# Performance work log

Measured on AMD Instinct MI355X. Metric: run time of the kernel, lower is better.

Reference implementation:

```python
import jax, jax.numpy as jnp
import numpy as np

B, D, P, OUT = 16384, 1024, 1024, 25


def setup_inputs() -> dict:
    key = jax.random.key(0)
    ks = jax.random.split(key, 8)
    return {
        "patient_embed": jax.random.normal(ks[0], (B, D), jnp.float32),
        "prototype_embed": jax.random.normal(ks[1], (P, D), jnp.float32),
        "index": jax.random.permutation(ks[2], B),
        "bilinear_w": jax.random.normal(ks[3], (1, D, D), jnp.float32) * 0.02,
        "bilinear_b": jnp.zeros((1,), jnp.float32),
        "lin_w": jax.random.normal(ks[4], (1, 2 * D), jnp.float32) * 0.02,
        "proto_fc_w": jax.random.normal(ks[5], (P, D), jnp.float32) * 0.02,
        "proto_fc_b": jnp.zeros((P,), jnp.float32),
        "class_fc_w": jax.random.normal(ks[6], (OUT, P), jnp.float32) * 0.02,
        "class_fc_b": jnp.zeros((OUT,), jnp.float32),
    }


def reference(patient_embed, prototype_embed, index, bilinear_w, bilinear_b,
              lin_w, proto_fc_w, proto_fc_b, class_fc_w, class_fc_b):
    # prototype codebook is detached in the original (clone().detach())
    protos = jax.lax.stop_gradient(prototype_embed)  # [P, D]

    # cdist + argmin: nearest prototype per patient (VQ-style codebook lookup)
    e_sq = jnp.sum(patient_embed * patient_embed, axis=-1, keepdims=True)  # [B,1]
    p_sq = jnp.sum(protos * protos, axis=-1)[None, :]                      # [1,P]
    d2 = e_sq + p_sq - 2.0 * (patient_embed @ protos.T)                    # [B,P]
    dist = jnp.sqrt(jnp.maximum(d2, 0.0))
    labels_a = jnp.argmin(dist, axis=1)                                    # [B]

    # mixup partner via permutation; its nearest prototype is a gather of labels_a
    embed_b = patient_embed[index]
    labels_b = labels_a[index]

    pa = protos[labels_a]  # [B, D] prototype gather
    pb = protos[labels_b]

    # BiaffineAttention: bilinear(pa, pb) + lin(cat(pa, pb))
    bil = jnp.einsum('bi,oij,bj->bo', pa, bilinear_w, pb) + bilinear_b     # [B,1]
    lin = jnp.concatenate([pa, pb], axis=1) @ lin_w.T                      # [B,1]
    lam = jax.nn.sigmoid(bil + lin)                                        # [B,1]

    # adaptive mixup blend
    mixed_embed = lam * patient_embed + (1.0 - lam) * embed_b              # [B,D]

    # class_linear(mixed_embed) = class_fc(leaky_relu(proto_fc(mixed_embed)))
    proto_logits = mixed_embed @ proto_fc_w.T + proto_fc_b                 # [B,P]
    cls_logits = jax.nn.leaky_relu(proto_logits, 0.01) @ class_fc_w.T + class_fc_b  # [B,OUT]
    return cls_logits
```

## Files before the change

### kernel.cpp

```cpp
#include <hip/hip_runtime.h>
#include <math.h>

#define B_   16384
#define D_   1024
#define P_   1024
#define KS_  2048
#define OUT_ 25
#define NT_  48

typedef unsigned short u16;
typedef unsigned int   u32;
typedef unsigned long long u64;
typedef __attribute__((ext_vector_type(8))) short short8;
typedef __attribute__((ext_vector_type(4))) float f32x4;
typedef _Float16 half_t;
typedef __attribute__((ext_vector_type(2))) _Float16 h2;

struct alignas(8) U16x4 { u16 x, y, z, w; };
struct alignas(8) H4 { half_t x, y, z, w; };
struct alignas(16) H8 { h2 a, b, c, d; };

#if defined(__has_builtin)
#if __has_builtin(__builtin_amdgcn_fdot2)
#define HAS_FDOT2 1
#endif
#endif

#define SBAR()  __builtin_amdgcn_s_barrier()
#define SFENCE() __builtin_amdgcn_sched_barrier(0)
#define WAITV8() asm volatile("s_waitcnt vmcnt(8)" ::: "memory")
#define WAITV0() asm volatile("s_waitcnt vmcnt(0)" ::: "memory")
#define WAITL0() asm volatile("s_waitcnt lgkmcnt(0)" ::: "memory")

__device__ __forceinline__ u16 f2bf(float f) {
  u32 u = __float_as_uint(f);
  u32 r = (u + 0x7FFFu + ((u >> 16) & 1u)) >> 16;
  return (u16)r;
}
__device__ __forceinline__ float bf2f(u16 h) {
  return __uint_as_float(((u32)h) << 16);
}
__device__ __forceinline__ u32 ordkey(float f) {
  u32 u = __float_as_uint(f);
  return (u & 0x80000000u) ? ~u : (u | 0x80000000u);
}
__device__ __forceinline__ void gload_lds16(const u16* g, u16* l) {
  __builtin_amdgcn_global_load_lds(
      (const __attribute__((address_space(1))) u32*)g,
      (__attribute__((address_space(3))) u32*)l, 16, 0, 0);
}
__device__ __forceinline__ float dot8(const H8& a, const H8& b, float c) {
#ifdef HAS_FDOT2
  c = __builtin_amdgcn_fdot2(a.a, b.a, c, false);
  c = __builtin_amdgcn_fdot2(a.b, b.b, c, false);
  c = __builtin_amdgcn_fdot2(a.c, b.c, c, false);
  c = __builtin_amdgcn_fdot2(a.d, b.d, c, false);
#else
  c += (float)a.a.x * (float)b.a.x + (float)a.a.y * (float)b.a.y;
  c += (float)a.b.x * (float)b.b.x + (float)a.b.y * (float)b.b.y;
  c += (float)a.c.x * (float)b.c.x + (float)a.c.y * (float)b.c.y;
  c += (float)a.d.x * (float)b.d.x + (float)a.d.y * (float)b.d.y;
#endif
  return c;
}
__device__ __forceinline__ int wrapNT(int t) { return t >= NT_ ? t - NT_ : t; }
__device__ __forceinline__ int acolf(int t) { t = wrapNT(t); return ((t >> 4) == 1 ? 1024 : 0) + (t & 15) * 64; }
__device__ __forceinline__ int bcolf(int t) { t = wrapNT(t); return ((t >> 4) == 2 ? 1024 : 0) + (t & 15) * 64; }


__global__ void conv_split(const float* __restrict__ in, u16* __restrict__ out) {
  int r = blockIdx.x, t = threadIdx.x;
  float4 x = ((const float4*)(in + (size_t)r * D_))[t];
  U16x4 h, l;
  h.x = f2bf(x.x); l.x = f2bf(x.x - bf2f(h.x));
  h.y = f2bf(x.y); l.y = f2bf(x.y - bf2f(h.y));
  h.z = f2bf(x.z); l.z = f2bf(x.z - bf2f(h.z));
  h.w = f2bf(x.w); l.w = f2bf(x.w - bf2f(h.w));
  u16* o = out + (size_t)r * KS_ + t * 4;
  *(U16x4*)(o)      = h;
  *(U16x4*)(o + D_) = l;
}

__global__ void convProtos(const float* __restrict__ protos, const float* __restrict__ lin_w,
                           u16* __restrict__ p2,
                           float* __restrict__ psq, float* __restrict__ uu, float* __restrict__ vv) {
  int r = blockIdx.x, t = threadIdx.x;
  float4 x  = ((const float4*)(protos + (size_t)r * D_))[t];
  float4 w1 = ((const float4*)(lin_w))[t];
  float4 w2 = ((const float4*)(lin_w + D_))[t];
  U16x4 h, l;
  h.x = f2bf(x.x); l.x = f2bf(x.x - bf2f(h.x));
  h.y = f2bf(x.y); l.y = f2bf(x.y - bf2f(h.y));
  h.z = f2bf(x.z); l.z = f2bf(x.z - bf2f(h.z));
  h.w = f2bf(x.w); l.w = f2bf(x.w - bf2f(h.w));
  u16* o = p2 + (size_t)r * KS_ + t * 4;
  *(U16x4*)(o) = h; *(U16x4*)(o + D_) = l;

  float s1 = x.x*x.x + x.y*x.y + x.z*x.z + x.w*x.w;
  float s2 = x.x*w1.x + x.y*w1.y + x.z*w1.z + x.w*w1.w;
  float s3 = x.x*w2.x + x.y*w2.y + x.z*w2.z + x.w*w2.w;
  #pragma unroll
  for (int mk = 1; mk < 64; mk <<= 1) {
    s1 += __shfl_xor(s1, mk);
    s2 += __shfl_xor(s2, mk);
    s3 += __shfl_xor(s3, mk);
  }
  __shared__ float r1[4], r2[4], r3[4];
  if ((t & 63) == 0) { int w = t >> 6; r1[w] = s1; r2[w] = s2; r3[w] = s3; }
  __syncthreads();
  if (t == 0) {
    psq[r] = r1[0] + r1[1] + r1[2] + r1[3];
    uu[r]  = r2[0] + r2[1] + r2[2] + r2[3];
    vv[r]  = r3[0] + r3[1] + r3[2] + r3[3];
  }
}

__global__ void convWt(const float* __restrict__ W, u16* __restrict__ wt2) {
  __shared__ float tile[64][65];
  int bx = blockIdx.x, by = blockIdx.y;
  int t = threadIdx.x;
  int c4 = (t & 15) * 4, r0 = t >> 4;
  #pragma unroll
  for (int rr = 0; rr < 64; rr += 16) {
    int r = rr + r0;
    float4 x = *(const float4*)(W + (size_t)(bx * 64 + r) * D_ + by * 64 + c4);
    tile[r][c4 + 0] = x.x; tile[r][c4 + 1] = x.y; tile[r][c4 + 2] = x.z; tile[r][c4 + 3] = x.w;
  }
  __syncthreads();
  #pragma unroll
  for (int rr = 0; rr < 64; rr += 16) {
    int r = rr + r0;
    U16x4 h, l;
    float v0 = tile[c4 + 0][r], v1 = tile[c4 + 1][r], v2 = tile[c4 + 2][r], v3 = tile[c4 + 3][r];
    h.x = f2bf(v0); l.x = f2bf(v0 - bf2f(h.x));
    h.y = f2bf(v1); l.y = f2bf(v1 - bf2f(h.y));
    h.z = f2bf(v2); l.z = f2bf(v2 - bf2f(h.z));
    h.w = f2bf(v3); l.w = f2bf(v3 - bf2f(h.w));
    u16* o = wt2 + (size_t)(by * 64 + r) * KS_ + bx * 64 + c4;
    *(U16x4*)(o) = h; *(U16x4*)(o + D_) = l;
  }
}

template<int MODE>
__global__ __launch_bounds__(512) void gemm256(
    const u16* __restrict__ A, const u16* __restrict__ Bm,
    u16* __restrict__ Ch,
    const float* __restrict__ psq, u64* __restrict__ packed,
    const float* __restrict__ bias)
{
  extern __shared__ u16 lds[];
  int bid = blockIdx.x;
  int wg = ((bid & 7) << 5) + (bid >> 3);
  int tm = wg >> 2, tn = wg & 3;
  int m0 = tm << 8, n0 = tn << 8;

  int tid = threadIdx.x;
  int w = tid >> 6, lane = tid & 63;
  int wm = w >> 2, wn = w & 3;
  int lr = lane & 15, lg = lane >> 4;

  #define AOFF(kkh, buf) (((kkh) * 2 + (buf)) * 8192)
  #define BOFF(kkh, buf) (32768 + ((kkh) * 2 + (buf)) * 8192)

  auto stage = [&](const u16* src, int row0, int colbase, int dstoff) {
    #pragma unroll
    for (int q = 0; q < 2; ++q) {
      int r = q * 128 + w * 16 + (lane >> 2);
      int c = ((lane & 3) * 8) ^ (((r >> 3) & 1) << 4);
      gload_lds16(src + (size_t)(row0 + r) * KS_ + colbase + c,
                  &lds[dstoff + q * 4096 + w * 512]);
    }
  };

  stage(A,  m0, acolf(0) +  0, AOFF(0, 0));
  stage(Bm, n0, bcolf(0) +  0, BOFF(0, 0));
  stage(A,  m0, acolf(0) + 32, AOFF(1, 0));
  stage(Bm, n0, bcolf(0) + 32, BOFF(1, 0));
  stage(A,  m0, acolf(1) +  0, AOFF(0, 1));
  stage(Bm, n0, bcolf(1) +  0, BOFF(0, 1));
  WAITV8();
  SBAR();

  f32x4 acc[8][4];
  #pragma unroll
  for (int i = 0; i < 8; ++i)
    #pragma unroll
    for (int j = 0; j < 4; ++j)
      acc[i][j] = (f32x4){0.f, 0.f, 0.f, 0.f};

  short8 bq[4];
  for (int t = 0; t < NT_; ++t) {
    int buf = t & 1;
    #pragma unroll
    for (int ph = 0; ph < 4; ++ph) {
      const int kkh = ph >> 1, mh = ph & 1;
      const u16* Asl = &lds[AOFF(kkh, buf)];
      const u16* Bsl = &lds[BOFF(kkh, buf)];
      short8 af[4];
      #pragma unroll
      for (int mi = 0; mi < 4; ++mi) {
        int r = wm * 128 + mh * 64 + mi * 16 + lr;
        af[mi] = *(const short8*)&Asl[r * 32 + ((lg * 8) ^ (((r >> 3) & 1) << 4))];
      }
      if (mh == 0) {
        #pragma unroll
        for (int nj = 0; nj < 4; ++nj) {
          int r = wn * 64 + nj * 16 + lr;
          bq[nj] = *(const short8*)&Bsl[r * 32 + ((lg * 8) ^ (((r >> 3) & 1) << 4))];
        }
      }
      if      (ph == 0) stage(A,  m0, acolf(t + 1) + 32, AOFF(1, (t + 1) & 1));
      else if (ph == 1) stage(Bm, n0, bcolf(t + 1) + 32, BOFF(1, (t + 1) & 1));
      else if (ph == 2) stage(A,  m0, acolf(t + 2) +  0, AOFF(0, buf));
      else              stage(Bm, n0, bcolf(t + 2) +  0, BOFF(0, buf));
      if (ph & 1) WAITV8();
      SBAR();
      WAITL0(); SFENCE();
      __builtin_amdgcn_s_setprio(1);
      #pragma unroll
      for (int mi = 0; mi < 4; ++mi)
        #pragma unroll
        for (int nj = 0; nj < 4; ++nj)
          acc[mh * 4 + mi][nj] =
            __builtin_amdgcn_mfma_f32_16x16x32_bf16(af[mi], bq[nj], acc[mh * 4 + mi][nj], 0, 0, 0);
      __builtin_amdgcn_s_setprio(0);
      SFENCE();
      SBAR();
    }
  }
  WAITV0();

  if (MODE == 1) {
    float pq[4];
    #pragma unroll
    for (int nj = 0; nj < 4; ++nj) pq[nj] = psq[n0 + wn * 64 + nj * 16 + lr];
    #pragma unroll
    for (int mi = 0; mi < 8; ++mi) {
      #pragma unroll
      for (int r = 0; r < 4; ++r) {
        float best = 1e30f; int bestn = 0x7fffffff;
        #pragma unroll
        for (int nj = 0; nj < 4; ++nj) {
          int n = n0 + wn * 64 + nj * 16 + lr;
          float d = pq[nj] - 2.0f * acc[mi][nj][r];
          if (d < best || (d == best && n < bestn)) { best = d; bestn = n; }
        }
        #pragma unroll
        for (int mk = 1; mk < 16; mk <<= 1) {
          float od = __shfl_xor(best, mk);
          int   on = __shfl_xor(bestn, mk);
          if (od < best || (od == best && on < bestn)) { best = od; bestn = on; }
        }
        if (lr == 0) {
          int m = m0 + wm * 128 + mi * 16 + lg * 4 + r;
          u64 key = ((u64)ordkey(best) << 32) | (u32)bestn;
          atomicMin(&packed[m], key);
        }
      }
    }
  } else {
    float bc[4];
    #pragma unroll
    for (int nj = 0; nj < 4; ++nj) bc[nj] = bias[n0 + wn * 64 + nj * 16 + lr];
    #pragma unroll
    for (int mi = 0; mi < 8; ++mi)
      #pragma unroll
      for (int nj = 0; nj < 4; ++nj)
        #pragma unroll
        for (int r = 0; r < 4; ++r) {
          int m = m0 + wm * 128 + mi * 16 + lg * 4 + r;
          int n = n0 + wn * 64 + nj * 16 + lr;
          float val = acc[mi][nj][r] + bc[nj];
          val = val >= 0.f ? val : 0.01f * val;
          half_t hv = (half_t)val;
          Ch[(size_t)m * P_ + n] = __builtin_bit_cast(u16, hv);
        }
  }
  #undef AOFF
  #undef BOFF
}

__global__ __launch_bounds__(256) void gemm_T_splitk(
    const u16* __restrict__ A, const u16* __restrict__ Bm, float* __restrict__ Cp)
{
  __shared__ u16 As[128 * 32];
  __shared__ u16 Bs[128 * 32];

  int bid = blockIdx.x;
  int swz = (bid & 7) * 24 + (bid >> 3);
  int kp = swz >> 6;
  int wg = swz & 63;
  int tm = wg >> 3, tn = wg & 7;
  int m0 = tm * 128, n0 = tn * 128;
  int abase = (kp == 1) ? 1024 : 0;
  int bbase = (kp == 2) ? 1024 : 0;

  int t = threadIdx.x;
  int w = t >> 6, lane = t & 63;
  int wr = w >> 1, wc = w & 1;
  int lr = lane & 15, lg = lane >> 4;

  const u16* src = (w < 2) ? A : Bm;
  int base_row = (w < 2) ? m0 : n0;
  int kbase = (w < 2) ? abase : bbase;
  int half = w & 1;
  int srow = base_row + half * 64 + (lane >> 2);
  int scol = (lane & 3) * 8;
  const u16* gsrc = src + (size_t)srow * KS_ + kbase + scol;
  u16* lbase = ((w < 2) ? As : Bs) + half * 2048;

  f32x4 acc[4][4];
  #pragma unroll
  for (int i = 0; i < 4; ++i)
    #pragma unroll
    for (int j = 0; j < 4; ++j)
      acc[i][j] = (f32x4){0.f, 0.f, 0.f, 0.f};

  for (int kt = 0; kt < 32; ++kt) {
    #pragma unroll
    for (int p = 0; p < 4; ++p)
      gload_lds16(gsrc + kt * 32 + (size_t)p * 16 * KS_, lbase + p * 512);
    __syncthreads();
    short8 af[4], bfr[4];
    #pragma unroll
    for (int i = 0; i < 4; ++i)
      af[i] = *(const short8*)&As[(wr * 64 + i * 16 + lr) * 32 + lg * 8];
    #pragma unroll
    for (int j = 0; j < 4; ++j)
      bfr[j] = *(const short8*)&Bs[(wc * 64 + j * 16 + lr) * 32 + lg * 8];
    #pragma unroll
    for (int i = 0; i < 4; ++i)
      #pragma unroll
      for (int j = 0; j < 4; ++j)
        acc[i][j] = __builtin_amdgcn_mfma_f32_16x16x32_bf16(af[i], bfr[j], acc[i][j], 0, 0, 0);
    __syncthreads();
  }

  float* Co = Cp + (size_t)kp * (P_ * D_);
  #pragma unroll
  for (int i = 0; i < 4; ++i)
    #pragma unroll
    for (int j = 0; j < 4; ++j)
      #pragma unroll
      for (int r = 0; r < 4; ++r) {
        int m = m0 + wr * 64 + i * 16 + lg * 4 + r;
        int n = n0 + wc * 64 + j * 16 + lr;
        Co[(size_t)m * D_ + n] = acc[i][j][r];
      }
}

__global__ void mix_kernel(const u64* __restrict__ packed, const int* __restrict__ index,
                           const float* __restrict__ Tp, const float* __restrict__ protos,
                           const float* __restrict__ patient,
                           const float* __restrict__ uu, const float* __restrict__ vv,
                           const float* __restrict__ bilb, u16* __restrict__ mixed2)
{
  int b = blockIdx.x, t = threadIdx.x;
  int la = (int)(packed[b] & 0xffffffffULL);
  int ib = index[b];
  int lb = (int)(packed[ib] & 0xffffffffULL);

  float4 t0 = ((const float4*)(Tp + (size_t)la * D_))[t];
  float4 t1 = ((const float4*)(Tp + (size_t)(P_ * D_) + (size_t)la * D_))[t];
  float4 t2 = ((const float4*)(Tp + (size_t)(2 * P_ * D_) + (size_t)la * D_))[t];
  float4 pb = ((const float4*)(protos + (size_t)lb * D_))[t];
  float tax = t0.x + t1.x + t2.x, tay = t0.y + t1.y + t2.y;
  float taz = t0.z + t1.z + t2.z, taw = t0.w + t1.w + t2.w;
  float part = tax*pb.x + tay*pb.y + taz*pb.z + taw*pb.w;
  #pragma unroll
  for (int mk = 1; mk < 64; mk <<= 1) part += __shfl_xor(part, mk);
  __shared__ float ws4[4];
  __shared__ float lamsh;
  if ((t & 63) == 0) ws4[t >> 6] = part;
  __syncthreads();
  if (t == 0) {
    float dot = ws4[0] + ws4[1] + ws4[2] + ws4[3];
    float z = dot + bilb[0] + uu[la] + vv[lb];
    lamsh = 1.0f / (1.0f + expf(-z));
  }
  __syncthreads();
  float lam = lamsh, oml = 1.0f - lam;

  float4 xa = ((const float4*)(patient + (size_t)b  * D_))[t];
  float4 xb = ((const float4*)(patient + (size_t)ib * D_))[t];
  float m0v = lam * xa.x + oml * xb.x;
  float m1v = lam * xa.y + oml * xb.y;
  float m2v = lam * xa.z + oml * xb.z;
  float m3v = lam * xa.w + oml * xb.w;
  U16x4 h, l;
  h.x = f2bf(m0v); l.x = f2bf(m0v - bf2f(h.x));
  h.y = f2bf(m1v); l.y = f2bf(m1v - bf2f(h.y));
  h.z = f2bf(m2v); l.z = f2bf(m2v - bf2f(h.z));
  h.w = f2bf(m3v); l.w = f2bf(m3v - bf2f(h.w));
  u16* o = mixed2 + (size_t)b * KS_ + t * 4;
  *(U16x4*)(o) = h; *(U16x4*)(o + D_) = l;
}

__global__ __launch_bounds__(256) void cls_kernel(const u16* __restrict__ pl,
                                                  const float* __restrict__ w,
                                                  const float* __restrict__ bias,
                                                  float* __restrict__ out)
{
  __shared__ half_t wl[25 * 1032];
  int t = threadIdx.x;
  for (int i = t; i < 25 * 256; i += 256) {
    float4 v = ((const float4*)w)[i];
    int o = i >> 8;
    int col = (i & 255) * 4;
    H4 hh; hh.x = (half_t)v.x; hh.y = (half_t)v.y; hh.z = (half_t)v.z; hh.w = (half_t)v.w;
    *(H4*)&wl[o * 1032 + col] = hh;
  }
  __syncthreads();

  int row = blockIdx.x * 64 + (t >> 2);
  int osub = t & 3;
  const H8* prow = (const H8*)(pl + (size_t)row * P_);
  float acc[7] = {0.f, 0.f, 0.f, 0.f, 0.f, 0.f, 0.f};

  for (int kk = 0; kk < 128; ++kk) {
    H8 a = prow[kk];
    #pragma unroll
    for (int j = 0; j < 7; ++j) {
      int o = 4 * j + osub;
      if (o < 25) {
        H8 wv = *(const H8*)&wl[o * 1032 + kk * 8];
        acc[j] = dot8(a, wv, acc[j]);
      }
    }
  }
  #pragma unroll
  for (int j = 0; j < 7; ++j) {
    int o = 4 * j + osub;
    if (o < 25) out[(size_t)row * OUT_ + o] = acc[j] + bias[o];
  }
}

extern "C" void kernel_launch(void* const* d_in, const int* in_sizes, int n_in,
                              void* d_out, int out_size, void* d_ws, size_t ws_size,
                              hipStream_t stream)
{
  const float* patient = (const float*)d_in[0];
  const float* protos  = (const float*)d_in[1];
  const int*   index   = (const int*)d_in[2];
  const float* W       = (const float*)d_in[3];
  const float* bilb    = (const float*)d_in[4];
  const float* lin_w   = (const float*)d_in[5];
  const float* pfc_w   = (const float*)d_in[6];
  const float* pfc_b   = (const float*)d_in[7];
  const float* cls_w   = (const float*)d_in[8];
  const float* cls_b   = (const float*)d_in[9];
  float* out = (float*)d_out;

  char* ws = (char*)d_ws;
  size_t off = 0;
  auto carve = [&](size_t bytes) -> char* {
    char* p = ws + off; off += (bytes + 255) & ~(size_t)255; return p;
  };
  u16* buf2   = (u16*)carve((size_t)B_ * KS_ * 2);
  u16* plh    = (u16*)carve((size_t)B_ * P_ * 2);
  u16* p2     = (u16*)carve((size_t)P_ * KS_ * 2);
  u16* pfc2   = (u16*)carve((size_t)P_ * KS_ * 2);
  u16* wt2    = (u16*)carve((size_t)D_ * KS_ * 2);
  float* Tp   = (float*)carve((size_t)3 * P_ * D_ * 4);
  u64* packed = (u64*)carve((size_t)B_ * 8);
  float* psq  = (float*)carve(P_ * 4);
  float* uu   = (float*)carve(P_ * 4);
  float* vv   = (float*)carve(P_ * 4);

  hipMemsetAsync(packed, 0xFF, (size_t)B_ * 8, stream);

  convProtos<<<P_, 256, 0, stream>>>(protos, lin_w, p2, psq, uu, vv);
  convWt<<<dim3(16, 16), 256, 0, stream>>>(W, wt2);
  conv_split<<<P_, 256, 0, stream>>>(pfc_w, pfc2);
  conv_split<<<B_, 256, 0, stream>>>(patient, buf2);

  gemm_T_splitk<<<192, 256, 0, stream>>>(p2, wt2, Tp);
  gemm256<1><<<256, 512, 131072, stream>>>(buf2, p2, nullptr, psq, packed, nullptr);
  mix_kernel<<<B_, 256, 0, stream>>>(packed, index, Tp, protos, patient, uu, vv, bilb, buf2);
  gemm256<2><<<256, 512, 131072, stream>>>(buf2, pfc2, plh, nullptr, nullptr, pfc_b);
  cls_kernel<<<256, 256, 0, stream>>>(plh, cls_w, cls_b, out);
}
```

Before: 431.7 us.

## Restructure GEMM main loop to whole-tile double buffering with two barriers

Replaces the four-phase per-iteration pipeline, which staged quarter tiles and hit two barriers per phase, with a simpler scheme. Each iteration issues all four global-to-LDS loads for the next K tile into the other buffer, waits, and runs four MFMA quarter blocks back to back with only two barriers. It also sets launch bounds to (512, 2) to ask for two workgroups per CU. The aim is to cut barrier count and synchronization stalls, at the cost of a shallower prefetch distance and possibly more register pressure.

```diff
diff --git a/kernel.cpp b/kernel.cpp
--- a/kernel.cpp
+++ b/kernel.cpp
@@ -26,11 +26,13 @@
 #endif
 #endif
 
-#define SBAR()  __builtin_amdgcn_s_barrier()
+#define SBAR()   __builtin_amdgcn_s_barrier()
 #define SFENCE() __builtin_amdgcn_sched_barrier(0)
 #define WAITV8() asm volatile("s_waitcnt vmcnt(8)" ::: "memory")
 #define WAITV0() asm volatile("s_waitcnt vmcnt(0)" ::: "memory")
 #define WAITL0() asm volatile("s_waitcnt lgkmcnt(0)" ::: "memory")
+#define PRIO1()  __builtin_amdgcn_s_setprio(1)
+#define PRIO0()  __builtin_amdgcn_s_setprio(0)
 
 __device__ __forceinline__ u16 f2bf(float f) {
   u32 u = __float_as_uint(f);
@@ -141,8 +143,19 @@
   }
 }
 
+#define MFMAQ(MH, AF, BQ)                                                        \
+  {                                                                              \
+    _Pragma("unroll")                                                            \
+    for (int mi = 0; mi < 4; ++mi) {                                             \
+      _Pragma("unroll")                                                          \
+      for (int nj = 0; nj < 4; ++nj)                                             \
+        acc[(MH) * 4 + mi][nj] = __builtin_amdgcn_mfma_f32_16x16x32_bf16(        \
+            (AF)[mi], (BQ)[nj], acc[(MH) * 4 + mi][nj], 0, 0, 0);                \
+    }                                                                            \
+  }
+
 template<int MODE>
-__global__ __launch_bounds__(512) void gemm256(
+__global__ __launch_bounds__(512, 2) void gemm256(
     const u16* __restrict__ A, const u16* __restrict__ Bm,
     u16* __restrict__ Ch,
     const float* __restrict__ psq, u64* __restrict__ packed,
@@ -171,15 +184,27 @@
                   &lds[dstoff + q * 4096 + w * 512]);
     }
   };
+  auto lda = [&](int kkh, int buf, int mh, short8* dst) {
+    const u16* Asl = &lds[AOFF(kkh, buf)];
+    #pragma unroll
+    for (int mi = 0; mi < 4; ++mi) {
+      int r = wm * 128 + mh * 64 + mi * 16 + lr;
+      dst[mi] = *(const short8*)&Asl[r * 32 + ((lg * 8) ^ (((r >> 3) & 1) << 4))];
+    }
+  };
+  auto ldb = [&](int kkh, int buf, short8* dst) {
+    const u16* Bsl = &lds[BOFF(kkh, buf)];
+    #pragma unroll
+    for (int nj = 0; nj < 4; ++nj) {
+      int r = wn * 64 + nj * 16 + lr;
+      dst[nj] = *(const short8*)&Bsl[r * 32 + ((lg * 8) ^ (((r >> 3) & 1) << 4))];
+    }
+  };
 
   stage(A,  m0, acolf(0) +  0, AOFF(0, 0));
+  stage(A,  m0, acolf(0) + 32, AOFF(1, 0));
   stage(Bm, n0, bcolf(0) +  0, BOFF(0, 0));
-  stage(A,  m0, acolf(0) + 32, AOFF(1, 0));
   stage(Bm, n0, bcolf(0) + 32, BOFF(1, 0));
-  stage(A,  m0, acolf(1) +  0, AOFF(0, 1));
-  stage(Bm, n0, bcolf(1) +  0, BOFF(0, 1));
-  WAITV8();
-  SBAR();
 
   f32x4 acc[8][4];
   #pragma unroll
@@ -188,45 +213,28 @@
     for (int j = 0; j < 4; ++j)
       acc[i][j] = (f32x4){0.f, 0.f, 0.f, 0.f};
 
-  short8 bq[4];
+  short8 af[4], bq[4];
   for (int t = 0; t < NT_; ++t) {
-    int buf = t & 1;
-    #pragma unroll
-    for (int ph = 0; ph < 4; ++ph) {
-      const int kkh = ph >> 1, mh = ph & 1;
-      const u16* Asl = &lds[AOFF(kkh, buf)];
-      const u16* Bsl = &lds[BOFF(kkh, buf)];
-      short8 af[4];
-      #pragma unroll
-      for (int mi = 0; mi < 4; ++mi) {
-        int r = wm * 128 + mh * 64 + mi * 16 + lr;
-        af[mi] = *(const short8*)&Asl[r * 32 + ((lg * 8) ^ (((r >> 3) & 1) << 4))];
-      }
-      if (mh == 0) {
-        #pragma unroll
-        for (int nj = 0; nj < 4; ++nj) {
-          int r = wn * 64 + nj * 16 + lr;
-          bq[nj] = *(const short8*)&Bsl[r * 32 + ((lg * 8) ^ (((r >> 3) & 1) << 4))];
-        }
-      }
-      if      (ph == 0) stage(A,  m0, acolf(t + 1) + 32, AOFF(1, (t + 1) & 1));
-      else if (ph == 1) stage(Bm, n0, bcolf(t + 1) + 32, BOFF(1, (t + 1) & 1));
-      else if (ph == 2) stage(A,  m0, acolf(t + 2) +  0, AOFF(0, buf));
-      else              stage(Bm, n0, bcolf(t + 2) +  0, BOFF(0, buf));
-      if (ph & 1) WAITV8();
-      SBAR();
-      WAITL0(); SFENCE();
-      __builtin_amdgcn_s_setprio(1);
-      #pragma unroll
-      for (int mi = 0; mi < 4; ++mi)
-        #pragma unroll
-        for (int nj = 0; nj < 4; ++nj)
-          acc[mh * 4 + mi][nj] =
-            __builtin_amdgcn_mfma_f32_16x16x32_bf16(af[mi], bq[nj], acc[mh * 4 + mi][nj], 0, 0, 0);
-      __builtin_amdgcn_s_setprio(0);
-      SFENCE();
-      SBAR();
-    }
+    int buf = t & 1, nbuf = buf ^ 1;
+    stage(A,  m0, acolf(t + 1) +  0, AOFF(0, nbuf));
+    stage(A,  m0, acolf(t + 1) + 32, AOFF(1, nbuf));
+    stage(Bm, n0, bcolf(t + 1) +  0, BOFF(0, nbuf));
+    stage(Bm, n0, bcolf(t + 1) + 32, BOFF(1, nbuf));
+    WAITV8();
+    SBAR();
+    lda(0, buf, 0, af); ldb(0, buf, bq);
+    WAITL0(); SFENCE();
+    PRIO1(); MFMAQ(0, af, bq); PRIO0(); SFENCE();
+    lda(0, buf, 1, af);
+    WAITL0(); SFENCE();
+    PRIO1(); MFMAQ(1, af, bq); PRIO0(); SFENCE();
+    lda(1, buf, 0, af); ldb(1, buf, bq);
+    WAITL0(); SFENCE();
+    PRIO1(); MFMAQ(0, af, bq); PRIO0(); SFENCE();
+    lda(1, buf, 1, af);
+    WAITL0(); SFENCE();
+    PRIO1(); MFMAQ(1, af, bq); PRIO0(); SFENCE();
+    SBAR();
   }
   WAITV0();
 
```

Result: slower. 442.8 us (+2.6%).
